# Performance work log

Measured on AMD Instinct MI355X. Metric: run time of the kernel, lower is better.

Reference implementation:

```python
import math
import jax, jax.numpy as jnp
import numpy as np

B, S, D, H = 4, 1024, 1024, 16
DK = D // H
NEG = jnp.float32(-1e32)
EPS = 1e-5


def setup_inputs() -> dict:
    key = jax.random.key(0)
    ks = jax.random.split(key, 10)
    s = 1.0 / math.sqrt(D)
    return {
        "query": jax.random.normal(ks[0], (B, S, D), jnp.float32),
        "key": jax.random.normal(ks[1], (B, S, D), jnp.float32),
        "values": jax.random.normal(ks[2], (B, S, D), jnp.float32),
        "lens": jax.random.randint(ks[3], (B,), 0, S).astype(jnp.int32),
        "state_weight": jax.random.normal(ks[4], (1, H, S, S), jnp.float32),
        # params (kq_same=True -> k shares q_linear weights)
        "Wq": jax.random.normal(ks[5], (D, D), jnp.float32) * s,
        "bq": jnp.zeros((D,), jnp.float32),
        "Wv": jax.random.normal(ks[6], (D, D), jnp.float32) * s,
        "bv": jnp.zeros((D,), jnp.float32),
        "Wo": jax.random.normal(ks[7], (D, D), jnp.float32) * s,
        "bo": jnp.zeros((D,), jnp.float32),
        "gamma": jnp.ones((D,), jnp.float32),
        "beta": jnp.zeros((D,), jnp.float32),
    }


def reference(query, key, values, lens, state_weight, Wq, bq, Wv, bv, Wo, bo, gamma, beta):
    # eval-mode forward of DTransformerLayer (peek_cur=False -> strictly causal)
    b, s, d = query.shape
    mask = jnp.tril(jnp.ones((s, s), bool), -1)[None, None]  # [1,1,S,S]

    q = (query @ Wq + bq).reshape(b, s, H, DK).transpose(0, 2, 1, 3)   # bhsd
    k = (key @ Wq + bq).reshape(b, s, H, DK).transpose(0, 2, 1, 3)     # shared weights (kq_same)
    v = (values @ Wv + bv).reshape(b, s, H, DK).transpose(0, 2, 1, 3)

    scores = jnp.einsum('bhqd,bhkd->bhqk', q, k) / math.sqrt(DK)
    scores = jnp.where(mask, scores, NEG)
    scores = jnp.where(mask, scores + state_weight, NEG)
    attn = jax.nn.softmax(scores, axis=-1)
    attn = jnp.where(mask, attn, 0.0)  # fully-masked rows (row 0) -> zeros, matching torch

    ctx = jnp.einsum('bhqk,bhkd->bhqd', attn, v).transpose(0, 2, 1, 3).reshape(b, s, d)
    out = ctx @ Wo + bo

    x = query + out  # dropout is identity in eval
    mu = jnp.mean(x, axis=-1, keepdims=True)
    var = jnp.mean(jnp.square(x - mu), axis=-1, keepdims=True)
    return (x - mu) * jax.lax.rsqrt(var + EPS) * gamma + beta
```

## Files before the change

### kernel.cpp

```cpp
#include <hip/hip_runtime.h>

#define B_ 4
#define S_ 1024
#define D_ 1024
#define H_ 16
#define DK_ 64

typedef __attribute__((ext_vector_type(8))) short short8;
typedef __attribute__((ext_vector_type(4))) float f32x4;
typedef __attribute__((ext_vector_type(16))) float f32x16;

#define QBPACK 0x7777666554433210ULL
#define T0PACK 0xC840A50605040000ULL
#define NTPACK 0x4444455665544642ULL
#define CBPACK  0x0C09070503020100ULL
#define NCHPACK 0x43222111U

static __device__ __forceinline__ unsigned bf16rne(float x) {
    unsigned b = __float_as_uint(x);
    return (b + 0x7FFFu + ((b >> 16) & 1u)) >> 16;
}

__global__ __launch_bounds__(256) void transpose_cvt3(
    const float* __restrict__ W0, const float* __restrict__ W1,
    const float* __restrict__ W2, ushort* __restrict__ T0,
    ushort* __restrict__ T1, ushort* __restrict__ T2)
{
    __shared__ float ts[32][33];
    const float* W = (blockIdx.z == 0) ? W0 : (blockIdx.z == 1) ? W1 : W2;
    ushort*     Wt = (blockIdx.z == 0) ? T0 : (blockIdx.z == 1) ? T1 : T2;
    const int t  = threadIdx.x;
    const int k0 = blockIdx.y * 32, n0 = blockIdx.x * 32;
    const int r  = t >> 3, c4 = (t & 7) * 4;
    const float4 v = *reinterpret_cast<const float4*>(&W[(size_t)(k0 + r) * 1024 + n0 + c4]);
    ts[r][c4] = v.x; ts[r][c4 + 1] = v.y; ts[r][c4 + 2] = v.z; ts[r][c4 + 3] = v.w;
    __syncthreads();
    ushort4 o;
    o.x = (ushort)bf16rne(ts[c4    ][r]);
    o.y = (ushort)bf16rne(ts[c4 + 1][r]);
    o.z = (ushort)bf16rne(ts[c4 + 2][r]);
    o.w = (ushort)bf16rne(ts[c4 + 3][r]);
    *reinterpret_cast<ushort4*>(&Wt[(size_t)(n0 + r) * 1024 + k0 + c4]) = o;
}

__global__ __launch_bounds__(256) void gemm_qkv(
    const float* __restrict__ q, const float* __restrict__ k,
    const float* __restrict__ v, const ushort* __restrict__ Wqt,
    const ushort* __restrict__ Wvt, const float* __restrict__ bq,
    const float* __restrict__ bv, ushort* __restrict__ Qh,
    ushort* __restrict__ Kh, ushort* __restrict__ Vt)
{
    __shared__ ushort As[2][64 * 64];
    __shared__ ushort Bs[2][128 * 64];

    const int t    = threadIdx.x;
    const int lane = t & 63;
    const int w    = t >> 6;

    const int cpx     = gridDim.x >> 3;
    const int logical = (blockIdx.x & 7) * cpx + (blockIdx.x >> 3);
    const int bm = logical >> 3;
    const int bn = logical & 7;

    const int mode = bm >> 6;
    const float* Xf = (mode == 0) ? q : (mode == 1) ? k : v;
    const ushort* Wt = (mode == 2) ? Wvt : Wqt;
    const float* bias = (mode == 2) ? bv : bq;
    const int rbase = (bm & 63) * 64;

    const int srow   = lane >> 3;
    const int schunk = (lane & 7) ^ srow;
    const float* ap[2];
#pragma unroll
    for (int j = 0; j < 2; ++j)
        ap[j] = Xf + (size_t)(rbase + (j * 4 + w) * 8 + srow) * 1024 + schunk * 8;

    const ushort* bg[4];
#pragma unroll
    for (int j = 0; j < 4; ++j)
        bg[j] = Wt + (size_t)(bn * 128 + (j * 4 + w) * 8 + srow) * 1024 + schunk * 8;

    float4 aRx0, aRy0, aRx1, aRy1;

#define A_ISSUE(k0)                                                              \
    do {                                                                         \
        aRx0 = *reinterpret_cast<const float4*>(ap[0] + (k0));                   \
        aRy0 = *reinterpret_cast<const float4*>(ap[0] + (k0) + 4);               \
        aRx1 = *reinterpret_cast<const float4*>(ap[1] + (k0));                   \
        aRy1 = *reinterpret_cast<const float4*>(ap[1] + (k0) + 4);               \
    } while (0)

#define B_STAGE(buf, k0)                                                         \
    do {                                                                         \
        _Pragma("unroll")                                                        \
        for (int j = 0; j < 4; ++j)                                              \
            __builtin_amdgcn_global_load_lds(                                    \
                (__attribute__((address_space(1))) const void*)(bg[j] + (k0)),   \
                (__attribute__((address_space(3))) void*)&Bs[buf][(j * 4 + w) * 512], \
                16, 0, 0);                                                       \
    } while (0)

#define A_WRITE(buf)                                                             \
    do {                                                                         \
        union { unsigned u[4]; int4 v; } p0, p1;                                 \
        asm("v_cvt_pk_bf16_f32 %0, %1, %2" : "=v"(p0.u[0]) : "v"(aRx0.x), "v"(aRx0.y)); \
        asm("v_cvt_pk_bf16_f32 %0, %1, %2" : "=v"(p0.u[1]) : "v"(aRx0.z), "v"(aRx0.w)); \
        asm("v_cvt_pk_bf16_f32 %0, %1, %2" : "=v"(p0.u[2]) : "v"(aRy0.x), "v"(aRy0.y)); \
        asm("v_cvt_pk_bf16_f32 %0, %1, %2" : "=v"(p0.u[3]) : "v"(aRy0.z), "v"(aRy0.w)); \
        asm("v_cvt_pk_bf16_f32 %0, %1, %2" : "=v"(p1.u[0]) : "v"(aRx1.x), "v"(aRx1.y)); \
        asm("v_cvt_pk_bf16_f32 %0, %1, %2" : "=v"(p1.u[1]) : "v"(aRx1.z), "v"(aRx1.w)); \
        asm("v_cvt_pk_bf16_f32 %0, %1, %2" : "=v"(p1.u[2]) : "v"(aRy1.x), "v"(aRy1.y)); \
        asm("v_cvt_pk_bf16_f32 %0, %1, %2" : "=v"(p1.u[3]) : "v"(aRy1.z), "v"(aRy1.w)); \
        *reinterpret_cast<int4*>(&As[buf][((0 * 4 + w) * 64 + lane) * 8]) = p0.v; \
        *reinterpret_cast<int4*>(&As[buf][((1 * 4 + w) * 64 + lane) * 8]) = p1.v; \
    } while (0)

    const int fr = lane & 15;
    const int fk = lane >> 4;
    const int wm = w >> 1, wn = w & 1;

    f32x4 acc[2][4];
#pragma unroll
    for (int m = 0; m < 2; ++m)
#pragma unroll
        for (int n = 0; n < 4; ++n) acc[m][n] = (f32x4){0.f, 0.f, 0.f, 0.f};

    A_ISSUE(0);
    B_STAGE(0, 0);
    asm volatile("s_waitcnt vmcnt(4)" ::: "memory");
    A_WRITE(0);
    asm volatile("s_waitcnt lgkmcnt(0)" ::: "memory");

#pragma unroll 1
    for (int kt = 0; kt < 16; ++kt) {
        const int cur = kt & 1;
        if (kt + 1 < 16) {
            A_ISSUE((kt + 1) * 64);
            B_STAGE(cur ^ 1, (kt + 1) * 64);
            asm volatile("s_waitcnt vmcnt(8)" ::: "memory");
        } else {
            asm volatile("s_waitcnt vmcnt(0)" ::: "memory");
        }
        __builtin_amdgcn_s_barrier();
        __builtin_amdgcn_sched_barrier(0);
#pragma unroll
        for (int ks = 0; ks < 2; ++ks) {
            short8 af[2], bf[4];
#pragma unroll
            for (int m = 0; m < 2; ++m) {
                const int row = wm * 32 + m * 16 + fr;
                af[m] = *reinterpret_cast<const short8*>(
                    &As[cur][row * 64 + (((ks * 4 + fk) ^ (row & 7)) * 8)]);
            }
#pragma unroll
            for (int n = 0; n < 4; ++n) {
                const int row = wn * 64 + n * 16 + fr;
                bf[n] = *reinterpret_cast<const short8*>(
                    &Bs[cur][row * 64 + (((ks * 4 + fk) ^ (row & 7)) * 8)]);
            }
            __builtin_amdgcn_s_setprio(1);
#pragma unroll
            for (int m = 0; m < 2; ++m)
#pragma unroll
                for (int n = 0; n < 4; ++n)
                    acc[m][n] = __builtin_amdgcn_mfma_f32_16x16x32_bf16(
                        af[m], bf[n], acc[m][n], 0, 0, 0);
            __builtin_amdgcn_s_setprio(0);
        }
        if (kt + 1 < 16) {
            asm volatile("s_waitcnt vmcnt(4)" ::: "memory");
            A_WRITE(cur ^ 1);
            asm volatile("s_waitcnt lgkmcnt(0)" ::: "memory");
        }
        __builtin_amdgcn_sched_barrier(0);
        __builtin_amdgcn_s_barrier();
        __builtin_amdgcn_sched_barrier(0);
    }
#undef A_ISSUE
#undef B_STAGE
#undef A_WRITE

#pragma unroll
    for (int m = 0; m < 2; ++m) {
        const int row0 = rbase + wm * 32 + m * 16 + fk * 4;
#pragma unroll
        for (int n = 0; n < 4; ++n) {
            const int col = bn * 128 + wn * 64 + n * 16 + fr;
            const float bc = bias[col];
            const int b_ = row0 >> 10, s0 = row0 & 1023;
            const int h  = col >> 6,   dk = col & 63;
            if (mode == 0) {
#pragma unroll
                for (int j = 0; j < 4; ++j)
                    Qh[(((size_t)b_ * H_ + h) * S_ + s0 + j) * DK_ + dk] =
                        (ushort)bf16rne((acc[m][n][j] + bc) * 0.125f);
            } else if (mode == 1) {
#pragma unroll
                for (int j = 0; j < 4; ++j)
                    Kh[(((size_t)b_ * H_ + h) * S_ + s0 + j) * DK_ + dk] =
                        (ushort)bf16rne(acc[m][n][j] + bc);
            } else {
                ushort4 pk;
                pk.x = (ushort)bf16rne(acc[m][n][0] + bc);
                pk.y = (ushort)bf16rne(acc[m][n][1] + bc);
                pk.z = (ushort)bf16rne(acc[m][n][2] + bc);
                pk.w = (ushort)bf16rne(acc[m][n][3] + bc);
                *reinterpret_cast<ushort4*>(
                    &Vt[(((size_t)b_ * H_ + h) * DK_ + dk) * S_ + s0]) = pk;
            }
        }
    }
}

__global__ __launch_bounds__(256) void gemm_bf16a(
    const ushort* __restrict__ X, const ushort* __restrict__ Wt,
    const float* __restrict__ bias, const float* __restrict__ resid,
    float* __restrict__ out)
{
    __shared__ ushort As[2][64 * 64];
    __shared__ ushort Bs[2][128 * 64];

    const int t    = threadIdx.x;
    const int lane = t & 63;
    const int w    = t >> 6;

    const int cpx     = gridDim.x >> 3;
    const int logical = (blockIdx.x & 7) * cpx + (blockIdx.x >> 3);
    const int bm = logical >> 3;
    const int bn = logical & 7;

    const int srow   = lane >> 3;
    const int schunk = (lane & 7) ^ srow;
    const ushort* ag[2];
    const ushort* bg[4];
#pragma unroll
    for (int j = 0; j < 2; ++j)
        ag[j] = X  + (size_t)(bm * 64 + (j * 4 + w) * 8 + srow) * 1024 + schunk * 8;
#pragma unroll
    for (int j = 0; j < 4; ++j)
        bg[j] = Wt + (size_t)(bn * 128 + (j * 4 + w) * 8 + srow) * 1024 + schunk * 8;

#define STAGE(buf, k0)                                                           \
    do {                                                                         \
        _Pragma("unroll")                                                        \
        for (int j = 0; j < 2; ++j)                                              \
            __builtin_amdgcn_global_load_lds(                                    \
                (__attribute__((address_space(1))) const void*)(ag[j] + (k0)),   \
                (__attribute__((address_space(3))) void*)&As[buf][(j * 4 + w) * 512], \
                16, 0, 0);                                                       \
        _Pragma("unroll")                                                        \
        for (int j = 0; j < 4; ++j)                                              \
            __builtin_amdgcn_global_load_lds(                                    \
                (__attribute__((address_space(1))) const void*)(bg[j] + (k0)),   \
                (__attribute__((address_space(3))) void*)&Bs[buf][(j * 4 + w) * 512], \
                16, 0, 0);                                                       \
    } while (0)

    const int fr = lane & 15;
    const int fk = lane >> 4;
    const int wm = w >> 1, wn = w & 1;

    f32x4 acc[2][4];
#pragma unroll
    for (int m = 0; m < 2; ++m)
#pragma unroll
        for (int n = 0; n < 4; ++n) acc[m][n] = (f32x4){0.f, 0.f, 0.f, 0.f};

    STAGE(0, 0);
#pragma unroll 1
    for (int kt = 0; kt < 16; ++kt) {
        const int cur = kt & 1;
        if (kt + 1 < 16) {
            STAGE(cur ^ 1, (kt + 1) * 64);
            asm volatile("s_waitcnt vmcnt(6)" ::: "memory");
        } else {
            asm volatile("s_waitcnt vmcnt(0)" ::: "memory");
        }
        __builtin_amdgcn_s_barrier();
        __builtin_amdgcn_sched_barrier(0);
#pragma unroll
        for (int ks = 0; ks < 2; ++ks) {
            short8 af[2], bf[4];
#pragma unroll
            for (int m = 0; m < 2; ++m) {
                const int row = wm * 32 + m * 16 + fr;
                af[m] = *reinterpret_cast<const short8*>(
                    &As[cur][row * 64 + (((ks * 4 + fk) ^ (row & 7)) * 8)]);
            }
#pragma unroll
            for (int n = 0; n < 4; ++n) {
                const int row = wn * 64 + n * 16 + fr;
                bf[n] = *reinterpret_cast<const short8*>(
                    &Bs[cur][row * 64 + (((ks * 4 + fk) ^ (row & 7)) * 8)]);
            }
            __builtin_amdgcn_s_setprio(1);
#pragma unroll
            for (int m = 0; m < 2; ++m)
#pragma unroll
                for (int n = 0; n < 4; ++n)
                    acc[m][n] = __builtin_amdgcn_mfma_f32_16x16x32_bf16(
                        af[m], bf[n], acc[m][n], 0, 0, 0);
            __builtin_amdgcn_s_setprio(0);
        }
        __builtin_amdgcn_sched_barrier(0);
        __builtin_amdgcn_s_barrier();
        __builtin_amdgcn_sched_barrier(0);
    }
#undef STAGE

#pragma unroll
    for (int m = 0; m < 2; ++m) {
        const int row0 = bm * 64 + wm * 32 + m * 16 + fk * 4;
#pragma unroll
        for (int n = 0; n < 4; ++n) {
            const int col = bn * 128 + wn * 64 + n * 16 + fr;
            const float bc = bias[col];
#pragma unroll
            for (int j = 0; j < 4; ++j) {
                const int row = row0 + j;
                out[(size_t)row * 1024 + col] =
                    acc[m][n][j] + bc + resid[(size_t)row * 1024 + col];
            }
        }
    }
}

__global__ __launch_bounds__(256) void attn_mfma(
    const ushort* __restrict__ Qh, const ushort* __restrict__ Kh,
    const ushort* __restrict__ Vt, const float* __restrict__ SW,
    ushort* __restrict__ ctxP, float2* __restrict__ ml)
{
    __shared__ ushort Ks[2][4096];
    __shared__ ushort Vs[2][4096];

    const int t    = threadIdx.x;
    const int lane = t & 63;
    const int w    = t >> 6;
    const int lg = (blockIdx.x & 7) * 128 + (blockIdx.x >> 3);
    const int b  = lg & 3;
    const int hc = lg >> 2;
    const int h  = hc >> 4;
    const int ci = hc & 15;
    const int bh = b * 16 + h;
    const int qb = (int)((QBPACK >> (ci * 4)) & 15);
    const int t0 = (int)((T0PACK >> (ci * 4)) & 15);
    const int nt = (int)((NTPACK >> (ci * 4)) & 15);

    const int ql = lane & 31;
    const int hi = lane >> 5;
    const int qrow = qb * 128 + ql * 4 + w;

    const ushort* Kg  = Kh + (size_t)bh * S_ * DK_;
    const ushort* Vg  = Vt + (size_t)bh * DK_ * S_;
    const float*  swp = SW + ((size_t)h * S_ + qrow) * S_;

    const ushort* kgp[2];
    const ushort* vgp[2];
#pragma unroll
    for (int j = 0; j < 2; ++j) {
        const int bb = w * 2 + j;
        const int g = bb >> 2, c = bb & 3;
        kgp[j] = Kg + (size_t)(g * 32 + ql) * DK_ + c * 16 + hi * 8;
        vgp[j] = Vg + (size_t)(g * 32 + ql) * S_  + c * 16 + hi * 8;
    }

#define ASTAGE(buf, k0)                                                          \
    do {                                                                         \
        _Pragma("unroll")                                                        \
        for (int j = 0; j < 2; ++j) {                                            \
            const int bb = w * 2 + j;                                            \
            __builtin_amdgcn_global_load_lds(                                    \
                (__attribute__((address_space(1))) const void*)(kgp[j] + (size_t)(k0) * DK_), \
                (__attribute__((address_space(3))) void*)&Ks[buf][bb * 512],     \
                16, 0, 0);                                                       \
            __builtin_amdgcn_global_load_lds(                                    \
                (__attribute__((address_space(1))) const void*)(vgp[j] + (k0)),  \
                (__attribute__((address_space(3))) void*)&Vs[buf][bb * 512],     \
                16, 0, 0);                                                       \
        }                                                                        \
    } while (0)

    short8 qf[4];
    {
        const ushort* Qg = Qh + ((size_t)bh * S_ + qrow) * DK_;
#pragma unroll
        for (int c = 0; c < 4; ++c) {
            union { int4 i; short8 s; } u;
            u.i = *reinterpret_cast<const int4*>(&Qg[c * 16 + hi * 8]);
            qf[c] = u.s;
        }
    }

    f32x16 accA, accB;
#pragma unroll
    for (int r = 0; r < 16; ++r) { accA[r] = 0.f; accB[r] = 0.f; }
    float mrow = -1e30f, lrow = 0.f;

    ASTAGE(0, t0 * 64);

#pragma unroll 1
    for (int kt = 0; kt < nt; ++kt) {
        const int cur = kt & 1;
        const int k0  = (t0 + kt) * 64;
        if (kt + 1 < nt) {
            ASTAGE(cur ^ 1, (t0 + kt + 1) * 64);
            asm volatile("s_waitcnt vmcnt(4)" ::: "memory");
        } else {
            asm volatile("s_waitcnt vmcnt(0)" ::: "memory");
        }
        __builtin_amdgcn_s_barrier();
        __builtin_amdgcn_sched_barrier(0);

        float swv[2][16];
#pragma unroll
        for (int g = 0; g < 2; ++g)
#pragma unroll
            for (int j = 0; j < 4; ++j) {
                const float4 v = *reinterpret_cast<const float4*>(
                    &swp[k0 + g * 32 + hi * 4 + j * 8]);
                swv[g][j * 4 + 0] = v.x; swv[g][j * 4 + 1] = v.y;
                swv[g][j * 4 + 2] = v.z; swv[g][j * 4 + 3] = v.w;
            }

        f32x16 sc[2];
        __builtin_amdgcn_s_setprio(1);
#pragma unroll
        for (int g = 0; g < 2; ++g) {
#pragma unroll
            for (int r = 0; r < 16; ++r) sc[g][r] = 0.f;
#pragma unroll
            for (int c = 0; c < 4; ++c) {
                const short8 kf = *reinterpret_cast<const short8*>(
                    &Ks[cur][((g * 4 + c) * 64 + lane) * 8]);
                sc[g] = __builtin_amdgcn_mfma_f32_32x32x16_bf16(kf, qf[c], sc[g], 0, 0, 0);
            }
        }
        __builtin_amdgcn_s_setprio(0);

        float pr[2][16];
        float tmax = -1e30f;
        if (t0 + kt >= 2 * qb) {
#pragma unroll
            for (int g = 0; g < 2; ++g)
#pragma unroll
                for (int r = 0; r < 16; ++r) {
                    const int key = k0 + g * 32 + (r & 3) + ((r >> 2) << 3) + (hi << 2);
                    const float s = (key < qrow) ? sc[g][r] + swv[g][r] : -1e30f;
                    pr[g][r] = s;
                    tmax = fmaxf(tmax, s);
                }
        } else {
#pragma unroll
            for (int g = 0; g < 2; ++g)
#pragma unroll
                for (int r = 0; r < 16; ++r) {
                    const float s = sc[g][r] + swv[g][r];
                    pr[g][r] = s;
                    tmax = fmaxf(tmax, s);
                }
        }
        tmax = fmaxf(tmax, __shfl_xor(tmax, 32, 64));
        const float mnew = fmaxf(mrow, tmax);
        const float corr = __expf(mrow - mnew);
        float psum = 0.f;
#pragma unroll
        for (int g = 0; g < 2; ++g)
#pragma unroll
            for (int r = 0; r < 16; ++r) {
                const float e = (pr[g][r] > -1e29f) ? __expf(pr[g][r] - mnew) : 0.f;
                pr[g][r] = e;
                psum += e;
            }
        psum += __shfl_xor(psum, 32, 64);
        lrow = lrow * corr + psum;
        mrow = mnew;
#pragma unroll
        for (int r = 0; r < 16; ++r) { accA[r] *= corr; accB[r] *= corr; }

        short8 paf[4];
#pragma unroll
        for (int g = 0; g < 2; ++g) {
            unsigned pk[8];
#pragma unroll
            for (int j = 0; j < 8; ++j) {
                unsigned r_;
                asm("v_cvt_pk_bf16_f32 %0, %1, %2"
                    : "=v"(r_) : "v"(pr[g][2 * j]), "v"(pr[g][2 * j + 1]));
                pk[j] = r_;
            }
            unsigned x0 = (unsigned)__shfl_xor((int)pk[0], 32, 64);
            unsigned x1 = (unsigned)__shfl_xor((int)pk[1], 32, 64);
            unsigned x2 = (unsigned)__shfl_xor((int)pk[2], 32, 64);
            unsigned x3 = (unsigned)__shfl_xor((int)pk[3], 32, 64);
            unsigned x4 = (unsigned)__shfl_xor((int)pk[4], 32, 64);
            unsigned x5 = (unsigned)__shfl_xor((int)pk[5], 32, 64);
            unsigned x6 = (unsigned)__shfl_xor((int)pk[6], 32, 64);
            unsigned x7 = (unsigned)__shfl_xor((int)pk[7], 32, 64);
            union { unsigned u[4]; short8 s; } a0, a1;
            a0.u[0] = hi ? x2 : pk[0];
            a0.u[1] = hi ? x3 : pk[1];
            a0.u[2] = hi ? pk[2] : x0;
            a0.u[3] = hi ? pk[3] : x1;
            a1.u[0] = hi ? x6 : pk[4];
            a1.u[1] = hi ? x7 : pk[5];
            a1.u[2] = hi ? pk[6] : x4;
            a1.u[3] = hi ? pk[7] : x5;
            paf[g * 2 + 0] = a0.s;
            paf[g * 2 + 1] = a1.s;
        }

        __builtin_amdgcn_s_setprio(1);
#pragma unroll
        for (int cc = 0; cc < 4; ++cc) {
            const short8 va = *reinterpret_cast<const short8*>(
                &Vs[cur][((0 * 4 + cc) * 64 + lane) * 8]);
            const short8 vb = *reinterpret_cast<const short8*>(
                &Vs[cur][((1 * 4 + cc) * 64 + lane) * 8]);
            accA = __builtin_amdgcn_mfma_f32_32x32x16_bf16(va, paf[cc], accA, 0, 0, 0);
            accB = __builtin_amdgcn_mfma_f32_32x32x16_bf16(vb, paf[cc], accB, 0, 0, 0);
        }
        __builtin_amdgcn_s_setprio(0);

        __builtin_amdgcn_sched_barrier(0);
        __builtin_amdgcn_s_barrier();
        __builtin_amdgcn_sched_barrier(0);
    }
#undef ASTAGE

    const float inv = (lrow > 0.f) ? 1.f / lrow : 0.f;
    ushort* crow_ = ctxP + ((size_t)(bh * 16 + ci) * 128 + (ql * 4 + w)) * 64;
#pragma unroll
    for (int g = 0; g < 4; ++g) {
        ushort4 oA, oB;
        oA.x = (ushort)bf16rne(accA[4 * g + 0] * inv);
        oA.y = (ushort)bf16rne(accA[4 * g + 1] * inv);
        oA.z = (ushort)bf16rne(accA[4 * g + 2] * inv);
        oA.w = (ushort)bf16rne(accA[4 * g + 3] * inv);
        oB.x = (ushort)bf16rne(accB[4 * g + 0] * inv);
        oB.y = (ushort)bf16rne(accB[4 * g + 1] * inv);
        oB.z = (ushort)bf16rne(accB[4 * g + 2] * inv);
        oB.w = (ushort)bf16rne(accB[4 * g + 3] * inv);
        *reinterpret_cast<ushort4*>(&crow_[g * 8 + hi * 4])      = oA;
        *reinterpret_cast<ushort4*>(&crow_[g * 8 + hi * 4 + 32]) = oB;
    }
    if (hi == 0) {
        float2 v; v.x = mrow; v.y = lrow;
        ml[(size_t)(bh * 16 + ci) * 128 + ql * 4 + w] = v;
    }
}

__global__ __launch_bounds__(256) void attn_merge(
    const ushort* __restrict__ ctxP, const float2* __restrict__ ml,
    ushort* __restrict__ ctx)
{
    const size_t idx = ((size_t)blockIdx.x * 256 + threadIdx.x) * 8;
    const int col = (int)(idx & 1023);
    const int row = (int)(idx >> 10);
    const int b = row >> 10, s = row & 1023;
    const int h = col >> 6, dk0 = col & 63;
    const int bh = b * 16 + h;
    const int qb = s >> 7, rl = s & 127;
    const int nch = (int)((NCHPACK >> (qb * 4)) & 15);
    const int cb  = (int)((CBPACK >> (qb * 8)) & 255);

    float mm[4], ll[4];
    float m = -1e30f;
#pragma unroll
    for (int c = 0; c < 4; ++c)
        if (c < nch) {
            const float2 v = ml[(size_t)(bh * 16 + cb + c) * 128 + rl];
            mm[c] = v.x; ll[c] = v.y;
            m = fmaxf(m, v.x);
        }
    float wc[4], wsum = 0.f;
#pragma unroll
    for (int c = 0; c < 4; ++c)
        if (c < nch) { wc[c] = ll[c] * __expf(mm[c] - m); wsum += wc[c]; }
    const float inv = (wsum > 0.f) ? 1.f / wsum : 0.f;

    float o[8] = {0.f, 0.f, 0.f, 0.f, 0.f, 0.f, 0.f, 0.f};
#pragma unroll
    for (int c = 0; c < 4; ++c)
        if (c < nch) {
            union { int4 v; ushort u[8]; } p;
            p.v = *reinterpret_cast<const int4*>(
                &ctxP[((size_t)(bh * 16 + cb + c) * 128 + rl) * 64 + dk0]);
            const float wgt = wc[c] * inv;
#pragma unroll
            for (int i = 0; i < 8; ++i)
                o[i] += wgt * __uint_as_float((unsigned)p.u[i] << 16);
        }
    union { int4 v; ushort u[8]; } r;
#pragma unroll
    for (int i = 0; i < 8; ++i) r.u[i] = (ushort)bf16rne(o[i]);
    *reinterpret_cast<int4*>(ctx + idx) = r.v;
}

__global__ __launch_bounds__(256) void layernorm_k(
    const float* __restrict__ x, const float* __restrict__ gamma,
    const float* __restrict__ beta, float* __restrict__ out)
{
    const int row = blockIdx.x;
    const int t   = threadIdx.x;
    const float4 v = *reinterpret_cast<const float4*>(&x[(size_t)row * D_ + (t << 2)]);
    float sum = v.x + v.y + v.z + v.w;
    float sq  = v.x * v.x + v.y * v.y + v.z * v.z + v.w * v.w;
#pragma unroll
    for (int w = 1; w < 64; w <<= 1) {
        sum += __shfl_xor(sum, w, 64);
        sq  += __shfl_xor(sq,  w, 64);
    }
    __shared__ float red[8];
    const int wid = t >> 6;
    if ((t & 63) == 0) { red[wid] = sum; red[wid + 4] = sq; }
    __syncthreads();
    sum = red[0] + red[1] + red[2] + red[3];
    sq  = red[4] + red[5] + red[6] + red[7];
    const float mu  = sum * (1.f / 1024.f);
    const float var = sq * (1.f / 1024.f) - mu * mu;
    const float rs  = rsqrtf(var + 1e-5f);
    const float4 gm = *reinterpret_cast<const float4*>(&gamma[t << 2]);
    const float4 bt = *reinterpret_cast<const float4*>(&beta[t << 2]);
    float4 o;
    o.x = (v.x - mu) * rs * gm.x + bt.x;
    o.y = (v.y - mu) * rs * gm.y + bt.y;
    o.z = (v.z - mu) * rs * gm.z + bt.z;
    o.w = (v.w - mu) * rs * gm.w + bt.w;
    *reinterpret_cast<float4*>(&out[(size_t)row * D_ + (t << 2)]) = o;
}

extern "C" void kernel_launch(void* const* d_in, const int* in_sizes, int n_in,
                              void* d_out, int out_size, void* d_ws, size_t ws_size,
                              hipStream_t stream)
{
    const float* query  = (const float*)d_in[0];
    const float* key    = (const float*)d_in[1];
    const float* values = (const float*)d_in[2];
    const float* SW     = (const float*)d_in[4];
    const float* Wq     = (const float*)d_in[5];
    const float* bq     = (const float*)d_in[6];
    const float* Wv     = (const float*)d_in[7];
    const float* bv     = (const float*)d_in[8];
    const float* Wo     = (const float*)d_in[9];
    const float* bo     = (const float*)d_in[10];
    const float* gamma  = (const float*)d_in[11];
    const float* beta   = (const float*)d_in[12];

    char* ws = (char*)d_ws;
    const size_t MB = 1024 * 1024;
    ushort* Qh   = (ushort*)(ws);
    ushort* Kh   = (ushort*)(ws +  8 * MB);
    ushort* Vt   = (ushort*)(ws + 16 * MB);
    ushort* Wqt  = (ushort*)(ws + 24 * MB);
    ushort* Wvt  = (ushort*)(ws + 26 * MB);
    ushort* Wot  = (ushort*)(ws + 28 * MB);
    ushort* ctxP = (ushort*)(ws + 30 * MB);
    float2* ml   = (float2*)(ws + 46 * MB);
    ushort* ctxm = Qh;
    float*  xbf  = (float*)(ws + 8 * MB);

    const dim3 blk(256);

    transpose_cvt3<<<dim3(32, 32, 3), blk, 0, stream>>>(Wq, Wv, Wo, Wqt, Wvt, Wot);

    gemm_qkv<<<dim3(1536), blk, 0, stream>>>(query, key, values, Wqt, Wvt,
                                             bq, bv, Qh, Kh, Vt);

    attn_mfma<<<dim3(1024), blk, 0, stream>>>(Qh, Kh, Vt, SW, ctxP, ml);
    attn_merge<<<dim3(2048), blk, 0, stream>>>(ctxP, ml, ctxm);

    gemm_bf16a<<<dim3(512), blk, 0, stream>>>(ctxm, Wot, bo, query, xbf);

    layernorm_k<<<dim3(4096), blk, 0, stream>>>(xbf, gamma, beta, (float*)d_out);
}
```

Before: 127.7 us.

## Deepen A-operand register prefetch to two stages in QKV projection GEMM

```diff
diff --git a/kernel.cpp b/kernel.cpp
--- a/kernel.cpp
+++ b/kernel.cpp
@@ -80,14 +80,23 @@
     for (int j = 0; j < 4; ++j)
         bg[j] = Wt + (size_t)(bn * 128 + (j * 4 + w) * 8 + srow) * 1024 + schunk * 8;
 
-    float4 aRx0, aRy0, aRx1, aRy1;
-
-#define A_ISSUE(k0)                                                              \
+    float4 s0x0, s0y0, s0x1, s0y1;
+    float4 s1x0, s1y0, s1x1, s1y1;
+
+#define A_ISSUE0(k0)                                                             \
     do {                                                                         \
-        aRx0 = *reinterpret_cast<const float4*>(ap[0] + (k0));                   \
-        aRy0 = *reinterpret_cast<const float4*>(ap[0] + (k0) + 4);               \
-        aRx1 = *reinterpret_cast<const float4*>(ap[1] + (k0));                   \
-        aRy1 = *reinterpret_cast<const float4*>(ap[1] + (k0) + 4);               \
+        s0x0 = *reinterpret_cast<const float4*>(ap[0] + (k0));                   \
+        s0y0 = *reinterpret_cast<const float4*>(ap[0] + (k0) + 4);               \
+        s0x1 = *reinterpret_cast<const float4*>(ap[1] + (k0));                   \
+        s0y1 = *reinterpret_cast<const float4*>(ap[1] + (k0) + 4);               \
+    } while (0)
+
+#define A_ISSUE1(k0)                                                             \
+    do {                                                                         \
+        s1x0 = *reinterpret_cast<const float4*>(ap[0] + (k0));                   \
+        s1y0 = *reinterpret_cast<const float4*>(ap[0] + (k0) + 4);               \
+        s1x1 = *reinterpret_cast<const float4*>(ap[1] + (k0));                   \
+        s1y1 = *reinterpret_cast<const float4*>(ap[1] + (k0) + 4);               \
     } while (0)
 
 #define B_STAGE(buf, k0)                                                         \
@@ -100,17 +109,17 @@
                 16, 0, 0);                                                       \
     } while (0)
 
-#define A_WRITE(buf)                                                             \
+#define A_WRITE_SET(buf, X0, Y0, X1, Y1)                                         \
     do {                                                                         \
         union { unsigned u[4]; int4 v; } p0, p1;                                 \
-        asm("v_cvt_pk_bf16_f32 %0, %1, %2" : "=v"(p0.u[0]) : "v"(aRx0.x), "v"(aRx0.y)); \
-        asm("v_cvt_pk_bf16_f32 %0, %1, %2" : "=v"(p0.u[1]) : "v"(aRx0.z), "v"(aRx0.w)); \
-        asm("v_cvt_pk_bf16_f32 %0, %1, %2" : "=v"(p0.u[2]) : "v"(aRy0.x), "v"(aRy0.y)); \
-        asm("v_cvt_pk_bf16_f32 %0, %1, %2" : "=v"(p0.u[3]) : "v"(aRy0.z), "v"(aRy0.w)); \
-        asm("v_cvt_pk_bf16_f32 %0, %1, %2" : "=v"(p1.u[0]) : "v"(aRx1.x), "v"(aRx1.y)); \
-        asm("v_cvt_pk_bf16_f32 %0, %1, %2" : "=v"(p1.u[1]) : "v"(aRx1.z), "v"(aRx1.w)); \
-        asm("v_cvt_pk_bf16_f32 %0, %1, %2" : "=v"(p1.u[2]) : "v"(aRy1.x), "v"(aRy1.y)); \
-        asm("v_cvt_pk_bf16_f32 %0, %1, %2" : "=v"(p1.u[3]) : "v"(aRy1.z), "v"(aRy1.w)); \
+        asm("v_cvt_pk_bf16_f32 %0, %1, %2" : "=v"(p0.u[0]) : "v"(X0.x), "v"(X0.y)); \
+        asm("v_cvt_pk_bf16_f32 %0, %1, %2" : "=v"(p0.u[1]) : "v"(X0.z), "v"(X0.w)); \
+        asm("v_cvt_pk_bf16_f32 %0, %1, %2" : "=v"(p0.u[2]) : "v"(Y0.x), "v"(Y0.y)); \
+        asm("v_cvt_pk_bf16_f32 %0, %1, %2" : "=v"(p0.u[3]) : "v"(Y0.z), "v"(Y0.w)); \
+        asm("v_cvt_pk_bf16_f32 %0, %1, %2" : "=v"(p1.u[0]) : "v"(X1.x), "v"(X1.y)); \
+        asm("v_cvt_pk_bf16_f32 %0, %1, %2" : "=v"(p1.u[1]) : "v"(X1.z), "v"(X1.w)); \
+        asm("v_cvt_pk_bf16_f32 %0, %1, %2" : "=v"(p1.u[2]) : "v"(Y1.x), "v"(Y1.y)); \
+        asm("v_cvt_pk_bf16_f32 %0, %1, %2" : "=v"(p1.u[3]) : "v"(Y1.z), "v"(Y1.w)); \
         *reinterpret_cast<int4*>(&As[buf][((0 * 4 + w) * 64 + lane) * 8]) = p0.v; \
         *reinterpret_cast<int4*>(&As[buf][((1 * 4 + w) * 64 + lane) * 8]) = p1.v; \
     } while (0)
@@ -125,60 +134,90 @@
 #pragma unroll
         for (int n = 0; n < 4; ++n) acc[m][n] = (f32x4){0.f, 0.f, 0.f, 0.f};
 
-    A_ISSUE(0);
+#define MFMA_TILE(buf)                                                           \
+    do {                                                                         \
+        _Pragma("unroll")                                                        \
+        for (int ks = 0; ks < 2; ++ks) {                                         \
+            short8 af[2], bf[4];                                                 \
+            _Pragma("unroll")                                                    \
+            for (int m = 0; m < 2; ++m) {                                        \
+                const int row = wm * 32 + m * 16 + fr;                           \
+                af[m] = *reinterpret_cast<const short8*>(                        \
+                    &As[buf][row * 64 + (((ks * 4 + fk) ^ (row & 7)) * 8)]);     \
+            }                                                                    \
+            _Pragma("unroll")                                                    \
+            for (int n = 0; n < 4; ++n) {                                        \
+                const int row = wn * 64 + n * 16 + fr;                           \
+                bf[n] = *reinterpret_cast<const short8*>(                        \
+                    &Bs[buf][row * 64 + (((ks * 4 + fk) ^ (row & 7)) * 8)]);     \
+            }                                                                    \
+            __builtin_amdgcn_s_setprio(1);                                       \
+            _Pragma("unroll")                                                    \
+            for (int m = 0; m < 2; ++m)                                          \
+                _Pragma("unroll")                                                \
+                for (int n = 0; n < 4; ++n)                                      \
+                    acc[m][n] = __builtin_amdgcn_mfma_f32_16x16x32_bf16(         \
+                        af[m], bf[n], acc[m][n], 0, 0, 0);                       \
+            __builtin_amdgcn_s_setprio(0);                                       \
+        }                                                                        \
+    } while (0)
+
+    A_ISSUE0(0);
+    A_ISSUE1(64);
     B_STAGE(0, 0);
-    asm volatile("s_waitcnt vmcnt(4)" ::: "memory");
-    A_WRITE(0);
+    asm volatile("s_waitcnt vmcnt(8)" ::: "memory");
+    A_WRITE_SET(0, s0x0, s0y0, s0x1, s0y1);
     asm volatile("s_waitcnt lgkmcnt(0)" ::: "memory");
+    __builtin_amdgcn_sched_barrier(0);
 
 #pragma unroll 1
-    for (int kt = 0; kt < 16; ++kt) {
-        const int cur = kt & 1;
-        if (kt + 1 < 16) {
-            A_ISSUE((kt + 1) * 64);
-            B_STAGE(cur ^ 1, (kt + 1) * 64);
-            asm volatile("s_waitcnt vmcnt(8)" ::: "memory");
-        } else {
-            asm volatile("s_waitcnt vmcnt(0)" ::: "memory");
-        }
+    for (int kt = 0; kt < 14; kt += 2) {
+        A_ISSUE0((kt + 2) * 64);
+        asm volatile("s_waitcnt vmcnt(4)" ::: "memory");
         __builtin_amdgcn_s_barrier();
         __builtin_amdgcn_sched_barrier(0);
-#pragma unroll
-        for (int ks = 0; ks < 2; ++ks) {
-            short8 af[2], bf[4];
-#pragma unroll
-            for (int m = 0; m < 2; ++m) {
-                const int row = wm * 32 + m * 16 + fr;
-                af[m] = *reinterpret_cast<const short8*>(
-                    &As[cur][row * 64 + (((ks * 4 + fk) ^ (row & 7)) * 8)]);
-            }
-#pragma unroll
-            for (int n = 0; n < 4; ++n) {
-                const int row = wn * 64 + n * 16 + fr;
-                bf[n] = *reinterpret_cast<const short8*>(
-                    &Bs[cur][row * 64 + (((ks * 4 + fk) ^ (row & 7)) * 8)]);
-            }
-            __builtin_amdgcn_s_setprio(1);
-#pragma unroll
-            for (int m = 0; m < 2; ++m)
-#pragma unroll
-                for (int n = 0; n < 4; ++n)
-                    acc[m][n] = __builtin_amdgcn_mfma_f32_16x16x32_bf16(
-                        af[m], bf[n], acc[m][n], 0, 0, 0);
-            __builtin_amdgcn_s_setprio(0);
-        }
-        if (kt + 1 < 16) {
-            asm volatile("s_waitcnt vmcnt(4)" ::: "memory");
-            A_WRITE(cur ^ 1);
-            asm volatile("s_waitcnt lgkmcnt(0)" ::: "memory");
-        }
+        B_STAGE(1, (kt + 1) * 64);
+        MFMA_TILE(0);
+        A_WRITE_SET(1, s1x0, s1y0, s1x1, s1y1);
+        asm volatile("s_waitcnt lgkmcnt(0)" ::: "memory");
         __builtin_amdgcn_sched_barrier(0);
         __builtin_amdgcn_s_barrier();
         __builtin_amdgcn_sched_barrier(0);
-    }
-#undef A_ISSUE
+
+        A_ISSUE1((kt + 3) * 64);
+        asm volatile("s_waitcnt vmcnt(4)" ::: "memory");
+        __builtin_amdgcn_s_barrier();
+        __builtin_amdgcn_sched_barrier(0);
+        B_STAGE(0, (kt + 2) * 64);
+        MFMA_TILE(1);
+        A_WRITE_SET(0, s0x0, s0y0, s0x1, s0y1);
+        asm volatile("s_waitcnt lgkmcnt(0)" ::: "memory");
+        __builtin_amdgcn_sched_barrier(0);
+        __builtin_amdgcn_s_barrier();
+        __builtin_amdgcn_sched_barrier(0);
+    }
+
+    asm volatile("s_waitcnt vmcnt(0)" ::: "memory");
+    __builtin_amdgcn_s_barrier();
+    __builtin_amdgcn_sched_barrier(0);
+    B_STAGE(1, 15 * 64);
+    MFMA_TILE(0);
+    A_WRITE_SET(1, s1x0, s1y0, s1x1, s1y1);
+    asm volatile("s_waitcnt lgkmcnt(0)" ::: "memory");
+    __builtin_amdgcn_sched_barrier(0);
+    __builtin_amdgcn_s_barrier();
+    __builtin_amdgcn_sched_barrier(0);
+
+    asm volatile("s_waitcnt vmcnt(0)" ::: "memory");
+    __builtin_amdgcn_s_barrier();
+    __builtin_amdgcn_sched_barrier(0);
+    MFMA_TILE(1);
+
+#undef A_ISSUE0
+#undef A_ISSUE1
 #undef B_STAGE
-#undef A_WRITE
+#undef A_WRITE_SET
+#undef MFMA_TILE
 
 #pragma unroll
     for (int m = 0; m < 2; ++m) {
```

After: 126.3 us. No clear change (-1.1%).

## Pre-convert QKV inputs to bf16 and use 128x128 tiles in QKV GEMM

Applied to the files above, without the earlier changes.

```diff
diff --git a/kernel.cpp b/kernel.cpp
--- a/kernel.cpp
+++ b/kernel.cpp
@@ -19,6 +19,29 @@
 static __device__ __forceinline__ unsigned bf16rne(float x) {
     unsigned b = __float_as_uint(x);
     return (b + 0x7FFFu + ((b >> 16) & 1u)) >> 16;
+}
+
+__global__ __launch_bounds__(256) void cvt3_bf16(
+    const float* __restrict__ q, const float* __restrict__ k,
+    const float* __restrict__ v, ushort* __restrict__ oq,
+    ushort* __restrict__ ok, ushort* __restrict__ ov)
+{
+    const size_t i = ((size_t)blockIdx.x * 256 + threadIdx.x) * 8;
+    const size_t FM = (size_t)4 * 1024 * 1024;
+    const float* in;
+    ushort* out;
+    size_t off;
+    if (i < FM)            { in = q; out = oq; off = i; }
+    else if (i < 2 * FM)   { in = k; out = ok; off = i - FM; }
+    else                   { in = v; out = ov; off = i - 2 * FM; }
+    const float4 a = *reinterpret_cast<const float4*>(in + off);
+    const float4 b = *reinterpret_cast<const float4*>(in + off + 4);
+    union { ushort u[8]; int4 vv; } p;
+    p.u[0] = (ushort)bf16rne(a.x); p.u[1] = (ushort)bf16rne(a.y);
+    p.u[2] = (ushort)bf16rne(a.z); p.u[3] = (ushort)bf16rne(a.w);
+    p.u[4] = (ushort)bf16rne(b.x); p.u[5] = (ushort)bf16rne(b.y);
+    p.u[6] = (ushort)bf16rne(b.z); p.u[7] = (ushort)bf16rne(b.w);
+    *reinterpret_cast<int4*>(out + off) = p.vv;
 }
 
 __global__ __launch_bounds__(256) void transpose_cvt3(
@@ -44,14 +67,14 @@
 }
 
 __global__ __launch_bounds__(256) void gemm_qkv(
-    const float* __restrict__ q, const float* __restrict__ k,
-    const float* __restrict__ v, const ushort* __restrict__ Wqt,
+    const ushort* __restrict__ qb_, const ushort* __restrict__ kb_,
+    const ushort* __restrict__ vb_, const ushort* __restrict__ Wqt,
     const ushort* __restrict__ Wvt, const float* __restrict__ bq,
     const float* __restrict__ bv, ushort* __restrict__ Qh,
     ushort* __restrict__ Kh, ushort* __restrict__ Vt)
 {
-    __shared__ ushort As[2][64 * 64];
-    __shared__ ushort Bs[2][128 * 64];
+    __shared__ ushort As[128 * 64];
+    __shared__ ushort Bs[128 * 64];
 
     const int t    = threadIdx.x;
     const int lane = t & 63;
@@ -62,127 +85,86 @@
     const int bm = logical >> 3;
     const int bn = logical & 7;
 
-    const int mode = bm >> 6;
-    const float* Xf = (mode == 0) ? q : (mode == 1) ? k : v;
+    const int mode = bm >> 5;
+    const ushort* Xb = (mode == 0) ? qb_ : (mode == 1) ? kb_ : vb_;
     const ushort* Wt = (mode == 2) ? Wvt : Wqt;
     const float* bias = (mode == 2) ? bv : bq;
-    const int rbase = (bm & 63) * 64;
+    const int rbase = (bm & 31) * 128;
 
     const int srow   = lane >> 3;
     const int schunk = (lane & 7) ^ srow;
-    const float* ap[2];
-#pragma unroll
-    for (int j = 0; j < 2; ++j)
-        ap[j] = Xf + (size_t)(rbase + (j * 4 + w) * 8 + srow) * 1024 + schunk * 8;
-
+    const ushort* ag[4];
     const ushort* bg[4];
 #pragma unroll
-    for (int j = 0; j < 4; ++j)
+    for (int j = 0; j < 4; ++j) {
+        ag[j] = Xb + (size_t)(rbase + (j * 4 + w) * 8 + srow) * 1024 + schunk * 8;
         bg[j] = Wt + (size_t)(bn * 128 + (j * 4 + w) * 8 + srow) * 1024 + schunk * 8;
-
-    float4 aRx0, aRy0, aRx1, aRy1;
-
-#define A_ISSUE(k0)                                                              \
-    do {                                                                         \
-        aRx0 = *reinterpret_cast<const float4*>(ap[0] + (k0));                   \
-        aRy0 = *reinterpret_cast<const float4*>(ap[0] + (k0) + 4);               \
-        aRx1 = *reinterpret_cast<const float4*>(ap[1] + (k0));                   \
-        aRy1 = *reinterpret_cast<const float4*>(ap[1] + (k0) + 4);               \
-    } while (0)
-
-#define B_STAGE(buf, k0)                                                         \
+    }
+
+#define STAGE(k0)                                                                \
     do {                                                                         \
         _Pragma("unroll")                                                        \
-        for (int j = 0; j < 4; ++j)                                              \
+        for (int j = 0; j < 4; ++j) {                                            \
+            __builtin_amdgcn_global_load_lds(                                    \
+                (__attribute__((address_space(1))) const void*)(ag[j] + (k0)),   \
+                (__attribute__((address_space(3))) void*)&As[(j * 4 + w) * 512], \
+                16, 0, 0);                                                       \
             __builtin_amdgcn_global_load_lds(                                    \
                 (__attribute__((address_space(1))) const void*)(bg[j] + (k0)),   \
-                (__attribute__((address_space(3))) void*)&Bs[buf][(j * 4 + w) * 512], \
+                (__attribute__((address_space(3))) void*)&Bs[(j * 4 + w) * 512], \
                 16, 0, 0);                                                       \
-    } while (0)
-
-#define A_WRITE(buf)                                                             \
-    do {                                                                         \
-        union { unsigned u[4]; int4 v; } p0, p1;                                 \
-        asm("v_cvt_pk_bf16_f32 %0, %1, %2" : "=v"(p0.u[0]) : "v"(aRx0.x), "v"(aRx0.y)); \
-        asm("v_cvt_pk_bf16_f32 %0, %1, %2" : "=v"(p0.u[1]) : "v"(aRx0.z), "v"(aRx0.w)); \
-        asm("v_cvt_pk_bf16_f32 %0, %1, %2" : "=v"(p0.u[2]) : "v"(aRy0.x), "v"(aRy0.y)); \
-        asm("v_cvt_pk_bf16_f32 %0, %1, %2" : "=v"(p0.u[3]) : "v"(aRy0.z), "v"(aRy0.w)); \
-        asm("v_cvt_pk_bf16_f32 %0, %1, %2" : "=v"(p1.u[0]) : "v"(aRx1.x), "v"(aRx1.y)); \
-        asm("v_cvt_pk_bf16_f32 %0, %1, %2" : "=v"(p1.u[1]) : "v"(aRx1.z), "v"(aRx1.w)); \
-        asm("v_cvt_pk_bf16_f32 %0, %1, %2" : "=v"(p1.u[2]) : "v"(aRy1.x), "v"(aRy1.y)); \
-        asm("v_cvt_pk_bf16_f32 %0, %1, %2" : "=v"(p1.u[3]) : "v"(aRy1.z), "v"(aRy1.w)); \
-        *reinterpret_cast<int4*>(&As[buf][((0 * 4 + w) * 64 + lane) * 8]) = p0.v; \
-        *reinterpret_cast<int4*>(&As[buf][((1 * 4 + w) * 64 + lane) * 8]) = p1.v; \
+        }                                                                        \
     } while (0)
 
     const int fr = lane & 15;
     const int fk = lane >> 4;
     const int wm = w >> 1, wn = w & 1;
 
-    f32x4 acc[2][4];
-#pragma unroll
-    for (int m = 0; m < 2; ++m)
+    f32x4 acc[4][4];
+#pragma unroll
+    for (int m = 0; m < 4; ++m)
 #pragma unroll
         for (int n = 0; n < 4; ++n) acc[m][n] = (f32x4){0.f, 0.f, 0.f, 0.f};
-
-    A_ISSUE(0);
-    B_STAGE(0, 0);
-    asm volatile("s_waitcnt vmcnt(4)" ::: "memory");
-    A_WRITE(0);
-    asm volatile("s_waitcnt lgkmcnt(0)" ::: "memory");
 
 #pragma unroll 1
     for (int kt = 0; kt < 16; ++kt) {
-        const int cur = kt & 1;
-        if (kt + 1 < 16) {
-            A_ISSUE((kt + 1) * 64);
-            B_STAGE(cur ^ 1, (kt + 1) * 64);
-            asm volatile("s_waitcnt vmcnt(8)" ::: "memory");
-        } else {
-            asm volatile("s_waitcnt vmcnt(0)" ::: "memory");
-        }
+        STAGE(kt * 64);
+        asm volatile("s_waitcnt vmcnt(0)" ::: "memory");
         __builtin_amdgcn_s_barrier();
         __builtin_amdgcn_sched_barrier(0);
 #pragma unroll
         for (int ks = 0; ks < 2; ++ks) {
-            short8 af[2], bf[4];
-#pragma unroll
-            for (int m = 0; m < 2; ++m) {
-                const int row = wm * 32 + m * 16 + fr;
+            short8 af[4], bf[4];
+#pragma unroll
+            for (int m = 0; m < 4; ++m) {
+                const int row = wm * 64 + m * 16 + fr;
                 af[m] = *reinterpret_cast<const short8*>(
-                    &As[cur][row * 64 + (((ks * 4 + fk) ^ (row & 7)) * 8)]);
+                    &As[row * 64 + (((ks * 4 + fk) ^ (row & 7)) * 8)]);
             }
 #pragma unroll
             for (int n = 0; n < 4; ++n) {
                 const int row = wn * 64 + n * 16 + fr;
                 bf[n] = *reinterpret_cast<const short8*>(
-                    &Bs[cur][row * 64 + (((ks * 4 + fk) ^ (row & 7)) * 8)]);
+                    &Bs[row * 64 + (((ks * 4 + fk) ^ (row & 7)) * 8)]);
             }
             __builtin_amdgcn_s_setprio(1);
 #pragma unroll
-            for (int m = 0; m < 2; ++m)
+            for (int m = 0; m < 4; ++m)
 #pragma unroll
                 for (int n = 0; n < 4; ++n)
                     acc[m][n] = __builtin_amdgcn_mfma_f32_16x16x32_bf16(
                         af[m], bf[n], acc[m][n], 0, 0, 0);
             __builtin_amdgcn_s_setprio(0);
         }
-        if (kt + 1 < 16) {
-            asm volatile("s_waitcnt vmcnt(4)" ::: "memory");
-            A_WRITE(cur ^ 1);
-            asm volatile("s_waitcnt lgkmcnt(0)" ::: "memory");
-        }
         __builtin_amdgcn_sched_barrier(0);
         __builtin_amdgcn_s_barrier();
         __builtin_amdgcn_sched_barrier(0);
     }
-#undef A_ISSUE
-#undef B_STAGE
-#undef A_WRITE
-
-#pragma unroll
-    for (int m = 0; m < 2; ++m) {
-        const int row0 = rbase + wm * 32 + m * 16 + fk * 4;
+#undef STAGE
+
+#pragma unroll
+    for (int m = 0; m < 4; ++m) {
+        const int row0 = rbase + wm * 64 + m * 16 + fk * 4;
 #pragma unroll
         for (int n = 0; n < 4; ++n) {
             const int col = bn * 128 + wn * 64 + n * 16 + fr;
@@ -656,15 +638,19 @@
     ushort* Wot  = (ushort*)(ws + 28 * MB);
     ushort* ctxP = (ushort*)(ws + 30 * MB);
     float2* ml   = (float2*)(ws + 46 * MB);
+    ushort* qbf  = (ushort*)(ws + 30 * MB);
+    ushort* kbf  = (ushort*)(ws + 38 * MB);
+    ushort* vbf  = (ushort*)(ws + 47 * MB);
     ushort* ctxm = Qh;
     float*  xbf  = (float*)(ws + 8 * MB);
 
     const dim3 blk(256);
 
+    cvt3_bf16<<<dim3(6144), blk, 0, stream>>>(query, key, values, qbf, kbf, vbf);
     transpose_cvt3<<<dim3(32, 32, 3), blk, 0, stream>>>(Wq, Wv, Wo, Wqt, Wvt, Wot);
 
-    gemm_qkv<<<dim3(1536), blk, 0, stream>>>(query, key, values, Wqt, Wvt,
-                                             bq, bv, Qh, Kh, Vt);
+    gemm_qkv<<<dim3(768), blk, 0, stream>>>(qbf, kbf, vbf, Wqt, Wvt,
+                                            bq, bv, Qh, Kh, Vt);
 
     attn_mfma<<<dim3(1024), blk, 0, stream>>>(Qh, Kh, Vt, SW, ctxP, ml);
     attn_merge<<<dim3(2048), blk, 0, stream>>>(ctxP, ml, ctxm);
```

After: 136.8 us. +7.2%, slower.
